# Optimization experiments

Measured on AMD Instinct MI355X. Metric: run time of the kernel, lower is better.

## Reference

```python
import jax, jax.numpy as jnp
import numpy as np

IGNORE_LABEL = -1.0
POS_THR, NEG_THR = 0.5, 0.4
BBOX_CLIP = float(np.log(1000.0 / 16.0))


def box_overlap(box, gt):
    # box [M,4], gt [G,4] -> IoU [M,G]  (legacy +1 box widths)
    area_b = (box[:, 2] - box[:, 0] + 1) * (box[:, 3] - box[:, 1] + 1)
    area_g = (gt[:, 2] - gt[:, 0] + 1) * (gt[:, 3] - gt[:, 1] + 1)
    iw = jnp.minimum(box[:, None, 2], gt[None, :, 2]) - jnp.maximum(box[:, None, 0], gt[None, :, 0]) + 1
    ih = jnp.minimum(box[:, None, 3], gt[None, :, 3]) - jnp.maximum(box[:, None, 1], gt[None, :, 1]) + 1
    inter = jnp.maximum(iw, 0.0) * jnp.maximum(ih, 0.0)
    union = area_b[:, None] + area_g[None, :] - inter
    return inter / jnp.maximum(union, 1.0)


def bbox_transform_inv(anchors, deltas):
    # decode deltas [M,4] against anchors [M,4]
    w = anchors[:, 2] - anchors[:, 0] + 1
    h = anchors[:, 3] - anchors[:, 1] + 1
    cx = anchors[:, 0] + 0.5 * w
    cy = anchors[:, 1] + 0.5 * h
    pcx = cx + deltas[:, 0] * w
    pcy = cy + deltas[:, 1] * h
    pw = w * jnp.exp(jnp.minimum(deltas[:, 2], BBOX_CLIP))
    ph = h * jnp.exp(jnp.minimum(deltas[:, 3], BBOX_CLIP))
    return jnp.stack([pcx - 0.5 * pw, pcy - 0.5 * ph, pcx + 0.5 * pw, pcy + 0.5 * ph], axis=1)


def bbox_transform(anchors, gt):
    # encode gt [M,4] against anchors [M,4]
    aw = anchors[:, 2] - anchors[:, 0] + 1
    ah = anchors[:, 3] - anchors[:, 1] + 1
    acx = anchors[:, 0] + 0.5 * aw
    acy = anchors[:, 1] + 0.5 * ah
    gw = gt[:, 2] - gt[:, 0] + 1
    gh = gt[:, 3] - gt[:, 1] + 1
    gcx = gt[:, 0] + 0.5 * gw
    gcy = gt[:, 1] + 0.5 * gh
    return jnp.stack([(gcx - acx) / aw, (gcy - acy) / ah, jnp.log(gw / aw), jnp.log(gh / ah)], axis=1)


def rpn_anchor_target(boxes, anchors4):
    # boxes [n,G,5] -> labels [n,A,2] (top-2 EMD matching), targets [n,2A,4]
    anc2 = jnp.repeat(anchors4, 2, axis=0)  # interleaved [a0,a0,a1,a1,...]
    def per_image(gt):
        ov = box_overlap(anchors4, gt[:, :4])                     # [A,G]
        valid = gt[:, 4] != IGNORE_LABEL
        ov = jnp.where(valid[None, :], ov, -1.0)
        vals, idx = jax.lax.top_k(ov, 2)                          # [A,2]
        labels = jnp.where(vals >= POS_THR, 1.0,
                           jnp.where(vals < NEG_THR, 0.0, IGNORE_LABEL))
        matched = gt[idx.reshape(-1), :4]                         # [2A,4]
        targets = bbox_transform(anc2, matched)
        return labels, targets
    return jax.vmap(per_image)(boxes)


def anchor_iou_target(boxes, anchors4, pred_reg):
    # decode both predictions per anchor, IoU vs gt, then best / 2nd-best match value
    A = anchors4.shape[0]
    anc2 = jnp.repeat(anchors4, 2, axis=0)
    def per_image(gt, off):
        off = off.reshape(-1, 4)                                  # [2A,4]
        dt = bbox_transform_inv(anc2, off)
        ov = box_overlap(dt, gt[:, :4])                           # [2A,G]
        keep = 1.0 - (gt[:, 4] == IGNORE_LABEL).astype(ov.dtype)
        ov = ov * keep[None, :]
        ov = ov.reshape(A, 2, -1)
        a, b = ov[:, 0, :], ov[:, 1, :]
        ia = jnp.argmax(a, axis=1)
        aval = jnp.take_along_axis(a, ia[:, None], axis=1)        # [A,1]
        b = b.at[jnp.arange(A), ia].set(0.0)                      # scatter best slot to 0
        ib = jnp.argmax(b, axis=1)
        bval = jnp.take_along_axis(b, ib[:, None], axis=1)
        return jnp.concatenate([aval, bval], axis=1)              # [A,2]
    return jax.vmap(per_image)(boxes, pred_reg)


def sigmoid_ce_retina(pred, label, alpha=0.25, gamma=2.0):
    # focal loss; pred [n,M,1] probs, label [n,M] in {-1,0,1}
    mask = (label != IGNORE_LABEL).astype(pred.dtype)
    vlabel = label * mask
    onehot = (vlabel == 1.0).astype(pred.dtype)[:, :, None]
    pos = (1.0 - pred) ** gamma * onehot * jnp.log(pred)
    neg = pred ** gamma * (1.0 - onehot) * jnp.log(1.0 - pred)
    loss = -(alpha * pos + (1.0 - alpha) * neg).sum(axis=2) * mask
    npos = jnp.maximum((label > 0).sum(), 1)
    return loss.sum() / npos


def fg_mask(label):
    # label not background(0) and not ignore(-1)
    return ((label != 0.0) & (label != IGNORE_LABEL)).astype(jnp.float32)


def smooth_l1_retina(pred, gt, label, sigma=3.0):
    s2 = sigma * sigma
    x = pred - gt
    ax = jnp.abs(x)
    val = jnp.where(ax < 1.0 / s2, 0.5 * s2 * x * x, ax - 0.5 / s2)
    mask = fg_mask(label)
    return (val.sum(axis=2) * mask).sum() / jnp.maximum(mask.sum(), 1.0)


def iou_l1(pred, target, label):
    mask = fg_mask(label)
    return (jnp.abs(pred - target) * mask).sum() / jnp.maximum(mask.sum(), 1.0)


def softmax_loss_fn(score, label):
    # score [M,c], label [M] ints with -1 = ignore
    logp = jax.nn.log_softmax(score, axis=1)
    mask = label != -1
    vlabel = jnp.where(mask, label, 0).astype(jnp.int32)
    picked = jnp.take_along_axis(logp, vlabel[:, None], axis=1)[:, 0]
    return -(picked * mask).sum() / jnp.maximum(mask.sum(), 1)


def setup_inputs() -> dict:
    key = jax.random.key(0)
    ks = jax.random.split(key, 10)
    n, A, G = 2, 120000, 300
    pred_cls = jax.nn.sigmoid(jax.random.normal(ks[0], (n, A, 2), jnp.float32))
    rpn_num_prob = jax.random.normal(ks[1], (n, A, 2), jnp.float32)
    pred_reg = 0.2 * jax.random.normal(ks[2], (n, A, 8), jnp.float32)
    rpn_iou = jax.nn.sigmoid(jax.random.normal(ks[3], (n, A, 2), jnp.float32))
    cx = jax.random.uniform(ks[4], (A,), minval=0.0, maxval=1024.0)
    cy = jax.random.uniform(ks[5], (A,), minval=0.0, maxval=1024.0)
    w = jax.random.uniform(ks[6], (A,), minval=16.0, maxval=256.0)
    h = jax.random.uniform(ks[7], (A,), minval=16.0, maxval=256.0)
    anchors = jnp.stack([cx - 0.5 * w, cy - 0.5 * h, cx + 0.5 * w, cy + 0.5 * h], axis=1)
    kx, ky, kw, kh, kl = jax.random.split(ks[8], 5)
    gx = jax.random.uniform(kx, (n, G), minval=0.0, maxval=900.0)
    gy = jax.random.uniform(ky, (n, G), minval=0.0, maxval=900.0)
    gw = jax.random.uniform(kw, (n, G), minval=20.0, maxval=200.0)
    gh = jax.random.uniform(kh, (n, G), minval=20.0, maxval=200.0)
    glab = jnp.where(jax.random.uniform(kl, (n, G)) < 0.95, 1.0, -1.0)
    boxes = jnp.stack([gx, gy, gx + gw, gy + gh, glab], axis=2)
    im_info = jnp.concatenate([
        jnp.tile(jnp.array([[1024.0, 1024.0, 1.0, 1024.0, 1024.0]], jnp.float32), (n, 1)),
        jnp.full((n, 1), float(G), jnp.float32)], axis=1)
    return {"pred_cls": pred_cls, "rpn_num_prob": rpn_num_prob, "pred_reg": pred_reg,
            "anchors": anchors, "rpn_iou": rpn_iou, "boxes": boxes, "im_info": im_info}


def reference(pred_cls, rpn_num_prob, pred_reg, anchors, rpn_iou, boxes, im_info):
    n = pred_cls.shape[0]
    anchors4 = anchors[:, :4]
    # anchor targets and iou targets are computed under no_grad in the original
    rpn_labels, rpn_target_boxes = jax.lax.stop_gradient(rpn_anchor_target(boxes, anchors4))
    ious_target = jax.lax.stop_gradient(anchor_iou_target(boxes, anchors4, pred_reg))
    target_boxes = rpn_target_boxes.reshape(n, -1, 4)   # [n,2A,4]
    cls_prob = pred_cls.reshape(n, -1, 1)               # [n,2A,1]
    offsets = pred_reg.reshape(n, -1, 4)                # [n,2A,4]
    a = rpn_labels[:, :, 0]
    b = rpn_labels[:, :, 1]
    ignores = b - (a == 0.0).astype(b.dtype) * (b != 0.0).astype(b.dtype)
    labels = jnp.stack([a, ignores], axis=2).reshape(n, -1)  # [n,2A]
    cls_loss = sigmoid_ce_retina(cls_prob, labels, 0.25, 2.0)
    bbox_loss = smooth_l1_retina(offsets, target_boxes, labels)
    lab2 = labels.reshape(n, -1, 2)
    iou_loss = iou_l1(rpn_iou, ious_target, lab2)
    nlabels = (lab2 > 0).sum(axis=2).reshape(-1).astype(jnp.int32) - 1  # in {-1,0,1}
    num_loss = softmax_loss_fn(rpn_num_prob.reshape(-1, rpn_num_prob.shape[2]), nlabels)
    # order: rpn_cls_loss, rpn_bbox_loss, rpn_iou_loss, rpn_num_loss
    return jnp.stack([cls_loss, 2.0 * bbox_loss, 2.0 * iou_loss, num_loss])
```

## Files before the change

### kernel.cpp

```cpp
#include <hip/hip_runtime.h>
#include <math.h>

#define G_MAX 384
#define O2S_MAX 512

#define XB 32
#define YB 16
#define NBINS 512
#define SCLX (32.0f / 900.0f)
#define SCLY (16.0f / 900.0f)

__device__ __forceinline__ int xbin(float v) {
  int b = (int)(v * SCLX);
  return min(max(b, 0), XB - 1);
}
__device__ __forceinline__ int ybin(float v) {
  int b = (int)(v * SCLY);
  return min(max(b, 0), YB - 1);
}

__device__ __forceinline__ float waveSum(float v) {
#pragma unroll
  for (int o = 32; o > 0; o >>= 1) v += __shfl_down(v, o, 64);
  return v;
}

__device__ __forceinline__ float huber9(float x) {
  float ax = fabsf(x);
  return (ax < (1.0f / 9.0f)) ? 4.5f * x * x : ax - (0.5f / 9.0f);
}

__device__ __forceinline__ float iouExact(float bx0, float by0, float bx1, float by1,
                                          float areab, float4 g, float areag) {
  float gx1 = g.z - 1.0f, gy1 = g.w - 1.0f;
  float iw = fminf(bx1, gx1) - fmaxf(bx0, g.x) + 1.0f;
  float ih = fminf(by1, gy1) - fmaxf(by0, g.y) + 1.0f;
  float inter = fmaxf(iw, 0.f) * fmaxf(ih, 0.f);
  float uni = areab + areag - inter;
  return inter / fmaxf(uni, 1.0f);
}

__device__ __forceinline__ uint32_t packKey(float x0, float y0, float x1p, float y1p,
                                            float area, float4 gb, float ga,
                                            uint32_t g) {
  float iw = fminf(x1p, gb.z) - fmaxf(x0, gb.x);
  float ih = fminf(y1p, gb.w) - fmaxf(y0, gb.y);
  float inter = fmaxf(iw, 0.f) * ih;
  float key = (area + ga) * __builtin_amdgcn_rcpf(inter);
  return (__float_as_uint(key) & 0xFFFFFE00u) | g;
}

__global__ __launch_bounds__(256) void retina_main(
    const float* __restrict__ pred_cls,
    const float* __restrict__ rpn_num,
    const float* __restrict__ pred_reg,
    const float* __restrict__ anchors,
    const float* __restrict__ rpn_iou,
    const float* __restrict__ boxes,
    int A, int G,
    double* __restrict__ partial)
{
  __shared__ float4 sBox[G_MAX];
  __shared__ float2 sMeta[G_MAX];
  __shared__ unsigned short sO2S[O2S_MAX];
  __shared__ int sCnt[NBINS];
  __shared__ int sStart[NBINS + 1];
  __shared__ int sWsum[4];
  __shared__ float sWaveMax[4][2];
  __shared__ float sSpanX, sSpanY;
  __shared__ float sRed[4][7];
  __shared__ float sStash[128][10];
  __shared__ float2 sRes[128];
  __shared__ unsigned char sList[128];
  __shared__ int sNum;

  const int img = blockIdx.y;
  const int seg = threadIdx.x & 1;
  const int duo = threadIdx.x >> 1;
  const int i   = blockIdx.x * 128 + duo;
  const int ic  = (i < A) ? i : (A - 1);
  const float* gtb = boxes + (size_t)img * G * 5;

  float4 a4 = *(const float4*)(anchors + (size_t)ic * 4);
  float ax0 = a4.x, ay0 = a4.y, ax1 = a4.z, ay1 = a4.w;
  float aw = ax1 - ax0 + 1.0f, ah = ay1 - ay0 + 1.0f;
  float areaa = aw * ah;
  float acx = ax0 + 0.5f * aw, acy = ay0 + 0.5f * ah;
  float ax1p = ax1 + 1.0f, ay1p = ay1 + 1.0f;

  float d0 = 0.f, d1 = 0.f, d2 = 0.f, d3 = 0.f;
  float d4 = 0.f, d5 = 0.f, d6 = 0.f, d7 = 0.f;
  float pcv0 = 0.f, pcv1 = 0.f, riv0 = 0.f, riv1 = 0.f, sn0 = 0.f, sn1 = 0.f;
  if (seg == 0) {
    const float* dp = pred_reg + ((size_t)img * A + ic) * 8;
    d0 = dp[0]; d1 = dp[1]; d2 = dp[2]; d3 = dp[3];
    d4 = dp[4]; d5 = dp[5]; d6 = dp[6]; d7 = dp[7];
    const float* pc = pred_cls + ((size_t)img * A + ic) * 2;
    pcv0 = pc[0]; pcv1 = pc[1];
    const float* ri = rpn_iou + ((size_t)img * A + ic) * 2;
    riv0 = ri[0]; riv1 = ri[1];
    const float* sp = rpn_num + ((size_t)img * A + ic) * 2;
    sn0 = sp[0]; sn1 = sp[1];
  }

  if (threadIdx.x == 0) sNum = 0;
  for (int b = threadIdx.x; b < NBINS; b += 256) sCnt[b] = 0;
  for (int s = G + threadIdx.x; s < G_MAX; s += 256) {
    sBox[s] = make_float4(0.f, 0.f, 1.f, 1.f);
    sMeta[s] = make_float2(1e30f, __uint_as_float((unsigned)s));
  }
  for (int s = G + threadIdx.x; s < O2S_MAX; s += 256)
    sO2S[s] = (unsigned short)G;
  __syncthreads();

  float rx0[2], ry0[2], rx1[2], ry1[2], rlb[2];
  int ng = 0;
  for (int g = threadIdx.x; g < G; g += 256, ++ng) {
    rx0[ng] = gtb[g * 5 + 0]; ry0[ng] = gtb[g * 5 + 1];
    rx1[ng] = gtb[g * 5 + 2]; ry1[ng] = gtb[g * 5 + 3];
    rlb[ng] = gtb[g * 5 + 4];
    atomicAdd(&sCnt[(ybin(ry0[ng]) << 5) | xbin(rx0[ng])], 1);
  }
  __syncthreads();

  {
    int t = threadIdx.x;
    int b0 = sCnt[t * 2 + 0], b1 = sCnt[t * 2 + 1];
    int tsum = b0 + b1;
    int lane = t & 63, wid = t >> 6;
    int incl = tsum;
#pragma unroll
    for (int o = 1; o < 64; o <<= 1) {
      int u = __shfl_up(incl, o, 64);
      if (lane >= o) incl += u;
    }
    if (lane == 63) sWsum[wid] = incl;
    __syncthreads();
    int woff = 0;
    for (int w = 0; w < wid; ++w) woff += sWsum[w];
    int excl = woff + incl - tsum;
    sStart[t * 2 + 0] = excl;
    sStart[t * 2 + 1] = excl + b0;
    if (t == 255) sStart[NBINS] = excl + tsum;
    sCnt[t * 2 + 0] = excl;
    sCnt[t * 2 + 1] = excl + b0;
  }
  __syncthreads();

  float mspanX = 0.f, mspanY = 0.f;
  {
    int g = threadIdx.x;
    for (int k = 0; k < ng; ++k, g += 256) {
      float x0 = rx0[k], y0 = ry0[k], x1 = rx1[k], y1 = ry1[k], lb = rlb[k];
      int pos = atomicAdd(&sCnt[(ybin(y0) << 5) | xbin(x0)], 1);
      float x1p = x1 + 1.0f, y1p = y1 + 1.0f;
      sBox[pos] = make_float4(x0, y0, x1p, y1p);
      sMeta[pos] = make_float2(
          (lb != -1.0f) ? (x1 - x0 + 1.0f) * (y1 - y0 + 1.0f) : 1e30f,
          __uint_as_float((unsigned)g));
      sO2S[g] = (unsigned short)pos;
      mspanX = fmaxf(mspanX, x1p - x0);
      mspanY = fmaxf(mspanY, y1p - y0);
    }
  }
#pragma unroll
  for (int m = 32; m > 0; m >>= 1) {
    mspanX = fmaxf(mspanX, __shfl_xor(mspanX, m, 64));
    mspanY = fmaxf(mspanY, __shfl_xor(mspanY, m, 64));
  }
  {
    int lane = threadIdx.x & 63, wid = threadIdx.x >> 6;
    if (lane == 0) { sWaveMax[wid][0] = mspanX; sWaveMax[wid][1] = mspanY; }
  }
  __syncthreads();
  if (threadIdx.x == 0) {
    sSpanX = fmaxf(fmaxf(sWaveMax[0][0], sWaveMax[1][0]),
                   fmaxf(sWaveMax[2][0], sWaveMax[3][0])) + 1.0f;
    sSpanY = fmaxf(fmaxf(sWaveMax[0][1], sWaveMax[1][1]),
                   fmaxf(sWaveMax[2][1], sWaveMax[3][1])) + 1.0f;
  }
  __syncthreads();
  const float spanX = sSpanX, spanY = sSpanY;

  float t_cls = 0.f, t_bbox = 0.f, t_iou = 0.f, t_num = 0.f;
  float t_npos = 0.f, t_nfg = 0.f, t_ncnt = 0.f;

  const float BBOX_CLIP = 4.1351666f;

  uint32_t an1 = 0xFFFFFFFFu, an2 = 0xFFFFFFFFu;
  {
    int xb0 = xbin(ax0 - spanX);
    int xb1 = xbin(ax1p);
    int yb0 = ybin(ay0 - spanY);
    int yb1 = ybin(ay1p);
    for (int yb = yb0; yb <= yb1; ++yb) {
      int lo = sStart[(yb << 5) + xb0];
      int hi = sStart[(yb << 5) + xb1 + 1];
#pragma unroll 2
      for (int s = lo + seg; s < hi; s += 2) {
        float4 gb = sBox[s];
        float2 mt = sMeta[s];
        uint32_t pk = packKey(ax0, ay0, ax1p, ay1p, areaa, gb, mt.x,
                              __float_as_uint(mt.y));
        uint32_t h = max(pk, an1);
        an1 = min(an1, pk);
        an2 = min(an2, h);
      }
    }
  }

  {
    uint32_t o1 = (uint32_t)__shfl_xor((int)an1, 1, 64);
    uint32_t o2 = (uint32_t)__shfl_xor((int)an2, 1, 64);
    uint32_t hi = max(an1, o1);
    an1 = min(an1, o1);
    an2 = min(min(an2, o2), hi);
  }

  bool fg0 = false, fg1 = false, needy = false;

  if (seg == 0 && i < A) {
    int og0 = (int)(an1 & 0x1FFu);
    int og1 = (int)(an2 & 0x1FFu);
    int s0 = sO2S[og0];
    int s1 = sO2S[og1];

    float4 g0 = sBox[s0]; float a0 = sMeta[s0].x; bool val0 = a0 < 1e29f;
    float v0 = val0 ? iouExact(ax0, ay0, ax1, ay1, areaa, g0, a0) : -1.0f;
    float4 g1 = sBox[s1]; float a1 = sMeta[s1].x; bool val1 = a1 < 1e29f;
    float v1 = val1 ? iouExact(ax0, ay0, ax1, ay1, areaa, g1, a1) : -1.0f;

    float la  = (v0 >= 0.5f) ? 1.0f : ((v0 < 0.4f) ? 0.0f : -1.0f);
    float lbv = (v1 >= 0.5f) ? 1.0f : ((v1 < 0.4f) ? 0.0f : -1.0f);
    float lab0 = la;
    float lab1 = lbv - (((la == 0.0f) && (lbv != 0.0f)) ? 1.0f : 0.0f);

    {
      float pv = pcv0;
      if (lab0 != -1.0f) {
        float l = (lab0 == 1.0f)
                      ? 0.25f * (1.0f - pv) * (1.0f - pv) * logf(pv)
                      : 0.75f * pv * pv * logf(1.0f - pv);
        t_cls -= l;
      }
      if (lab0 > 0.f) t_npos += 1.f;
      float qv = pcv1;
      if (lab1 != -1.0f) {
        float l = (lab1 == 1.0f)
                      ? 0.25f * (1.0f - qv) * (1.0f - qv) * logf(qv)
                      : 0.75f * qv * qv * logf(1.0f - qv);
        t_cls -= l;
      }
      if (lab1 > 0.f) t_npos += 1.f;
    }

    fg0 = (lab0 != 0.0f) && (lab0 != -1.0f);
    fg1 = (lab1 != 0.0f) && (lab1 != -1.0f);

    float raw = __builtin_amdgcn_rcpf(aw), rah = __builtin_amdgcn_rcpf(ah);

    if (fg0) {
      float mx1 = g0.z - 1.0f, my1 = g0.w - 1.0f;
      float gw = mx1 - g0.x + 1.0f, gh = my1 - g0.y + 1.0f;
      float gcx = g0.x + 0.5f * gw, gcy = g0.y + 0.5f * gh;
      float t0 = (gcx - acx) * raw, t1v = (gcy - acy) * rah;
      float t2 = logf(gw * raw), t3 = logf(gh * rah);
      t_bbox += huber9(d0 - t0) + huber9(d1 - t1v) + huber9(d2 - t2) + huber9(d3 - t3);
      t_nfg += 1.f;
    }
    if (fg1) {
      float mx1 = g1.z - 1.0f, my1 = g1.w - 1.0f;
      float gw = mx1 - g1.x + 1.0f, gh = my1 - g1.y + 1.0f;
      float gcx = g1.x + 0.5f * gw, gcy = g1.y + 0.5f * gh;
      float t0 = (gcx - acx) * raw, t1v = (gcy - acy) * rah;
      float t2 = logf(gw * raw), t3 = logf(gh * rah);
      t_bbox += huber9(d4 - t0) + huber9(d5 - t1v) + huber9(d6 - t2) + huber9(d7 - t3);
      t_nfg += 1.f;
    }

    {
      int nl = ((lab0 > 0.f) ? 1 : 0) + ((lab1 > 0.f) ? 1 : 0) - 1;
      if (nl != -1) {
        float m = fmaxf(sn0, sn1);
        float lse = m + logf(expf(sn0 - m) + expf(sn1 - m));
        float picked = ((nl == 0) ? sn0 : sn1) - lse;
        t_num -= picked;
        t_ncnt += 1.f;
      }
    }

    needy = fg0 || fg1;
    if (needy) {
      float p0cx = acx + d0 * aw, p0cy = acy + d1 * ah;
      float p0w = aw * expf(fminf(d2, BBOX_CLIP));
      float p0h = ah * expf(fminf(d3, BBOX_CLIP));
      float b0x0 = p0cx - 0.5f * p0w, b0y0 = p0cy - 0.5f * p0h;
      float b0x1 = p0cx + 0.5f * p0w, b0y1 = p0cy + 0.5f * p0h;
      float area0 = (b0x1 - b0x0 + 1.0f) * (b0y1 - b0y0 + 1.0f);

      float p1cx = acx + d4 * aw, p1cy = acy + d5 * ah;
      float p1w = aw * expf(fminf(d6, BBOX_CLIP));
      float p1h = ah * expf(fminf(d7, BBOX_CLIP));
      float b1x0 = p1cx - 0.5f * p1w, b1y0 = p1cy - 0.5f * p1h;
      float b1x1 = p1cx + 0.5f * p1w, b1y1 = p1cy + 0.5f * p1h;
      float area1 = (b1x1 - b1x0 + 1.0f) * (b1y1 - b1y0 + 1.0f);

      int slot = atomicAdd(&sNum, 1);
      sList[slot] = (unsigned char)duo;
      float* st = sStash[slot];
      st[0] = b0x0; st[1] = b0y0; st[2] = b0x1; st[3] = b0y1; st[4] = area0;
      st[5] = b1x0; st[6] = b1y0; st[7] = b1x1; st[8] = b1y1; st[9] = area1;
    }
  }
  __syncthreads();

  {
    int num = sNum;
    for (int sb = 0; sb < num; sb += 64) {
      int slot = sb + (threadIdx.x >> 2);
      int wseg = threadIdx.x & 3;
      if (slot < num) {
        const float* st = sStash[slot];
        float c0x0 = st[0], c0y0 = st[1], c0x1 = st[2], c0y1 = st[3], car0 = st[4];
        float c1x0 = st[5], c1y0 = st[6], c1x1 = st[7], c1y1 = st[8], car1 = st[9];
        float c0x1p = c0x1 + 1.0f, c0y1p = c0y1 + 1.0f;
        float c1x1p = c1x1 + 1.0f, c1y1p = c1y1 + 1.0f;

        uint32_t am = 0xFFFFFFFFu;
        uint32_t bk1 = 0xFFFFFFFFu, bk2 = 0xFFFFFFFFu;

        int xb0 = xbin(fminf(c0x0, c1x0) - spanX);
        int xb1 = xbin(fmaxf(c0x1p, c1x1p));
        int yb0 = ybin(fminf(c0y0, c1y0) - spanY);
        int yb1 = ybin(fmaxf(c0y1p, c1y1p));
        for (int yb = yb0; yb <= yb1; ++yb) {
          int lo = sStart[(yb << 5) + xb0];
          int hi = sStart[(yb << 5) + xb1 + 1];
#pragma unroll 2
          for (int s = lo + wseg; s < hi; s += 4) {
            float4 gb = sBox[s];
            float2 mt = sMeta[s];
            uint32_t og = __float_as_uint(mt.y);
            am = min(am, packKey(c0x0, c0y0, c0x1p, c0y1p, car0, gb, mt.x, og));
            uint32_t pk = packKey(c1x0, c1y0, c1x1p, c1y1p, car1, gb, mt.x, og);
            uint32_t hib = max(pk, bk1);
            bk1 = min(bk1, pk);
            bk2 = min(bk2, hib);
          }
        }

#pragma unroll
        for (int m = 1; m <= 2; m <<= 1) {
          am = min(am, (uint32_t)__shfl_xor((int)am, m, 64));
          uint32_t q1 = (uint32_t)__shfl_xor((int)bk1, m, 64);
          uint32_t q2 = (uint32_t)__shfl_xor((int)bk2, m, 64);
          uint32_t hib = max(bk1, q1);
          bk1 = min(bk1, q1);
          bk2 = min(min(bk2, q2), hib);
        }

        if (wseg == 0) {
          int ai  = (int)(am  & 0x1FFu);
          int bi  = (int)(bk1 & 0x1FFu);
          int bi2 = (int)(bk2 & 0x1FFu);
          int sa = sO2S[ai];
          float4 ga4 = sBox[sa]; float aav = sMeta[sa].x;
          float aval = (aav < 1e29f) ? iouExact(c0x0, c0y0, c0x1, c0y1, car0, ga4, aav) : 0.0f;
          int bIdx = (ai == bi) ? bi2 : bi;
          int sb2 = sO2S[bIdx];
          float4 gb4 = sBox[sb2]; float abv = sMeta[sb2].x;
          float bval = (abv < 1e29f) ? iouExact(c1x0, c1y0, c1x1, c1y1, car1, gb4, abv) : 0.0f;
          sRes[sList[slot]] = make_float2(aval, bval);
        }
      }
    }
  }
  __syncthreads();

  if (needy) {
    float2 r = sRes[duo];
    if (fg0) t_iou += fabsf(riv0 - r.x);
    if (fg1) t_iou += fabsf(riv1 - fmaxf(r.y, 0.0f));
  }

  float vals[7] = {t_cls, t_bbox, t_iou, t_num, t_npos, t_nfg, t_ncnt};
  int lane = threadIdx.x & 63;
  int wid = threadIdx.x >> 6;
#pragma unroll
  for (int k = 0; k < 7; ++k) {
    float s = waveSum(vals[k]);
    if (lane == 0) sRed[wid][k] = s;
  }
  __syncthreads();
  if (threadIdx.x < 7) {
    double s = (double)sRed[0][threadIdx.x] + (double)sRed[1][threadIdx.x] +
               (double)sRed[2][threadIdx.x] + (double)sRed[3][threadIdx.x];
    size_t bid = (size_t)blockIdx.y * gridDim.x + blockIdx.x;
    partial[bid * 8 + threadIdx.x] = s;
  }
}

__global__ __launch_bounds__(1024) void retina_finalize(
    const double* __restrict__ partial, int nB, float* __restrict__ out) {
  __shared__ double sRed[16][7];
  double loc[7] = {0.0, 0.0, 0.0, 0.0, 0.0, 0.0, 0.0};
  for (int b = threadIdx.x; b < nB; b += 1024) {
    const double* r = partial + (size_t)b * 8;
#pragma unroll
    for (int k = 0; k < 7; ++k) loc[k] += r[k];
  }
  int lane = threadIdx.x & 63;
  int wid = threadIdx.x >> 6;
#pragma unroll
  for (int k = 0; k < 7; ++k) {
    double v = loc[k];
#pragma unroll
    for (int o = 32; o > 0; o >>= 1) v += __shfl_down(v, o, 64);
    if (lane == 0) sRed[wid][k] = v;
  }
  __syncthreads();
  if (threadIdx.x == 0) {
    double t[7];
#pragma unroll
    for (int k = 0; k < 7; ++k) {
      double s = 0.0;
      for (int w = 0; w < 16; ++w) s += sRed[w][k];
      t[k] = s;
    }
    double dpos = t[4] > 1.0 ? t[4] : 1.0;
    double dfg  = t[5] > 1.0 ? t[5] : 1.0;
    double dcnt = t[6] > 1.0 ? t[6] : 1.0;
    out[0] = (float)(t[0] / dpos);
    out[1] = (float)(2.0 * t[1] / dfg);
    out[2] = (float)(2.0 * t[2] / dfg);
    out[3] = (float)(t[3] / dcnt);
  }
}

extern "C" void kernel_launch(void* const* d_in, const int* in_sizes, int n_in,
                              void* d_out, int out_size, void* d_ws, size_t ws_size,
                              hipStream_t stream) {
  const float* pred_cls = (const float*)d_in[0];
  const float* rpn_num  = (const float*)d_in[1];
  const float* pred_reg = (const float*)d_in[2];
  const float* anchors  = (const float*)d_in[3];
  const float* rpn_iou  = (const float*)d_in[4];
  const float* boxes    = (const float*)d_in[5];

  int A = in_sizes[3] / 4;
  int n = in_sizes[0] / (2 * A);
  int G = in_sizes[5] / (5 * n);

  double* partial = (double*)d_ws;

  int nBx = (A + 127) / 128;
  int nB = nBx * n;
  dim3 grid(nBx, n, 1);
  retina_main<<<grid, dim3(256, 1, 1), 0, stream>>>(
      pred_cls, rpn_num, pred_reg, anchors, rpn_iou, boxes, A, G, partial);
  retina_finalize<<<dim3(1, 1, 1), dim3(1024, 1, 1), 0, stream>>>(
      partial, nB, (float*)d_out);
}
```

Before: 128.4 us.

## Assign one anchor per thread instead of two threads per anchor

Each thread now owns a single anchor and scans its whole candidate GT range itself, where before two threads split the scan and merged their top-2 keys with a shuffle. Blocks cover 256 anchors, so the grid halves and the per-block GT setup (bin counting, prefix sums, shared box staging) is amortized over twice as many anchors. The cost is a longer serial inner loop per thread and larger stash arrays, which may lower latency hiding and occupancy.

Result: faster. 119.8 us (-6.7%).

```diff
diff --git a/kernel.cpp b/kernel.cpp
--- a/kernel.cpp
+++ b/kernel.cpp
@@ -69,15 +69,14 @@
   __shared__ float sWaveMax[4][2];
   __shared__ float sSpanX, sSpanY;
   __shared__ float sRed[4][7];
-  __shared__ float sStash[128][10];
-  __shared__ float2 sRes[128];
-  __shared__ unsigned char sList[128];
+  __shared__ float sStash[256][10];
+  __shared__ float2 sRes[256];
+  __shared__ unsigned char sList[256];
   __shared__ int sNum;
 
   const int img = blockIdx.y;
-  const int seg = threadIdx.x & 1;
-  const int duo = threadIdx.x >> 1;
-  const int i   = blockIdx.x * 128 + duo;
+  const int own = threadIdx.x;
+  const int i   = blockIdx.x * 256 + own;
   const int ic  = (i < A) ? i : (A - 1);
   const float* gtb = boxes + (size_t)img * G * 5;
 
@@ -88,20 +87,15 @@
   float acx = ax0 + 0.5f * aw, acy = ay0 + 0.5f * ah;
   float ax1p = ax1 + 1.0f, ay1p = ay1 + 1.0f;
 
-  float d0 = 0.f, d1 = 0.f, d2 = 0.f, d3 = 0.f;
-  float d4 = 0.f, d5 = 0.f, d6 = 0.f, d7 = 0.f;
-  float pcv0 = 0.f, pcv1 = 0.f, riv0 = 0.f, riv1 = 0.f, sn0 = 0.f, sn1 = 0.f;
-  if (seg == 0) {
-    const float* dp = pred_reg + ((size_t)img * A + ic) * 8;
-    d0 = dp[0]; d1 = dp[1]; d2 = dp[2]; d3 = dp[3];
-    d4 = dp[4]; d5 = dp[5]; d6 = dp[6]; d7 = dp[7];
-    const float* pc = pred_cls + ((size_t)img * A + ic) * 2;
-    pcv0 = pc[0]; pcv1 = pc[1];
-    const float* ri = rpn_iou + ((size_t)img * A + ic) * 2;
-    riv0 = ri[0]; riv1 = ri[1];
-    const float* sp = rpn_num + ((size_t)img * A + ic) * 2;
-    sn0 = sp[0]; sn1 = sp[1];
-  }
+  const float* dp = pred_reg + ((size_t)img * A + ic) * 8;
+  float d0 = dp[0], d1 = dp[1], d2 = dp[2], d3 = dp[3];
+  float d4 = dp[4], d5 = dp[5], d6 = dp[6], d7 = dp[7];
+  const float* pc = pred_cls + ((size_t)img * A + ic) * 2;
+  float pcv0 = pc[0], pcv1 = pc[1];
+  const float* ri = rpn_iou + ((size_t)img * A + ic) * 2;
+  float riv0 = ri[0], riv1 = ri[1];
+  const float* sp = rpn_num + ((size_t)img * A + ic) * 2;
+  float sn0 = sp[0], sn1 = sp[1];
 
   if (threadIdx.x == 0) sNum = 0;
   for (int b = threadIdx.x; b < NBINS; b += 256) sCnt[b] = 0;
@@ -197,7 +191,7 @@
       int lo = sStart[(yb << 5) + xb0];
       int hi = sStart[(yb << 5) + xb1 + 1];
 #pragma unroll 2
-      for (int s = lo + seg; s < hi; s += 2) {
+      for (int s = lo; s < hi; ++s) {
         float4 gb = sBox[s];
         float2 mt = sMeta[s];
         uint32_t pk = packKey(ax0, ay0, ax1p, ay1p, areaa, gb, mt.x,
@@ -209,17 +203,9 @@
     }
   }
 
-  {
-    uint32_t o1 = (uint32_t)__shfl_xor((int)an1, 1, 64);
-    uint32_t o2 = (uint32_t)__shfl_xor((int)an2, 1, 64);
-    uint32_t hi = max(an1, o1);
-    an1 = min(an1, o1);
-    an2 = min(min(an2, o2), hi);
-  }
-
   bool fg0 = false, fg1 = false, needy = false;
 
-  if (seg == 0 && i < A) {
+  if (i < A) {
     int og0 = (int)(an1 & 0x1FFu);
     int og1 = (int)(an2 & 0x1FFu);
     int s0 = sO2S[og0];
@@ -306,7 +292,7 @@
       float area1 = (b1x1 - b1x0 + 1.0f) * (b1y1 - b1y0 + 1.0f);
 
       int slot = atomicAdd(&sNum, 1);
-      sList[slot] = (unsigned char)duo;
+      sList[slot] = (unsigned char)own;
       float* st = sStash[slot];
       st[0] = b0x0; st[1] = b0y0; st[2] = b0x1; st[3] = b0y1; st[4] = area0;
       st[5] = b1x0; st[6] = b1y0; st[7] = b1x1; st[8] = b1y1; st[9] = area1;
@@ -378,7 +364,7 @@
   __syncthreads();
 
   if (needy) {
-    float2 r = sRes[duo];
+    float2 r = sRes[own];
     if (fg0) t_iou += fabsf(riv0 - r.x);
     if (fg1) t_iou += fabsf(riv1 - fmaxf(r.y, 0.0f));
   }
@@ -453,7 +439,7 @@
 
   double* partial = (double*)d_ws;
 
-  int nBx = (A + 127) / 128;
+  int nBx = (A + 255) / 256;
   int nB = nBx * n;
   dim3 grid(nBx, n, 1);
   retina_main<<<grid, dim3(256, 1, 1), 0, stream>>>(
```
